# Performance work log

Measured on AMD Instinct MI355X. Metric: run time of the kernel, lower is better.

The kernel has to match this reference:

```python
import jax, jax.numpy as jnp
import numpy as np

PI_APPROX = 3.14  # the original module uses 3.14, not math.pi
FPS = 30.0        # hard-coded sampling rate in calc_hr_torch


def setup_inputs() -> dict:
    key = jax.random.key(0)
    x = jax.random.normal(key, (4096, 4096), dtype=jnp.float32)
    return {"x": x}


def reference(x) -> jnp.ndarray:
    test_n, sig_length = x.shape
    # mean-subtract each signal (over last dim)
    x = x - jnp.mean(x, axis=-1, keepdims=True)

    # custom_fft: DFT over dim 0 (size test_n), O(N^2) via trig matmuls
    N = test_n
    n = jnp.arange(N, dtype=jnp.float32)[:, None]  # [N,1]
    k = jnp.arange(N, dtype=jnp.float32)[None, :]  # [1,N]
    ang = (-2.0 * PI_APPROX / N) * (k * n)         # [N,N]
    real_part = jnp.matmul(jnp.cos(ang), x)        # [N, sig_length]
    imag_part = jnp.matmul(jnp.sin(ang), x)

    # custom_rfft: keep non-negative frequencies along dim 0
    half = N // 2 + 1 if N % 2 == 0 else (N + 1) // 2
    real_part = real_part[:half]
    imag_part = imag_part[:half]

    Ns = sig_length
    freq = jnp.arange(Ns, dtype=jnp.float32) / (Ns / FPS)  # [sig_length]
    amplitude = jnp.sqrt(real_part ** 2 + imag_part ** 2) / Ns  # [half, sig_length]
    hr_list = freq[jnp.argmax(amplitude, axis=-1)] * 60.0       # [half]
    return hr_list
```

## Files before the change

kernel.cpp:

```cpp
#include <hip/hip_runtime.h>
#include <cmath>

typedef _Float16 f16;
typedef _Float16 f16x8 __attribute__((ext_vector_type(8)));
typedef float f32x4 __attribute__((ext_vector_type(4)));
typedef unsigned long long u64;

#define M_OUT 2049
#define NDIM 4096
#define MPAD 2112
#define CW ((float)(-2.0 * 3.14 / 4096.0))

static const size_t WS_MEAN  = 0;
static const size_t WS_CELLS = 16384;
static const size_t WS_TBL   = 40960;
static const size_t A_ELEMS  = (size_t)MPAD * NDIM;
static const size_t X_ELEMS  = (size_t)NDIM * NDIM;
static const size_t WS_XTBL  = WS_TBL + 4 * A_ELEMS * sizeof(f16);
static const size_t WS_FULL_END = WS_XTBL + 2 * X_ELEMS * sizeof(f16);
static const size_t WS_MID_END  = WS_TBL + 4 * A_ELEMS * sizeof(f16);

#define AS1 __attribute__((address_space(1)))
#define AS3 __attribute__((address_space(3)))
__device__ __forceinline__ void async_copy16(const void* gsrc, void* ldst) {
    __builtin_amdgcn_global_load_lds((const AS1 unsigned int*)gsrc,
                                     (AS3 unsigned int*)ldst, 16, 0, 0);
}

__device__ __forceinline__ void split_f16(float v, f16& hi, f16& lo) {
    hi = (f16)v;
    lo = (f16)((v - (float)hi) * 64.0f);
}

__global__ void mean_kernel(const float* __restrict__ x, float* __restrict__ meanv) {
    const int row = blockIdx.x;
    const float4* xr = (const float4*)(x + (size_t)row * NDIM);
    float s = 0.f;
    for (int i = threadIdx.x; i < NDIM / 4; i += 256) {
        float4 v = xr[i];
        s += (v.x + v.y) + (v.z + v.w);
    }
    for (int off = 32; off; off >>= 1) s += __shfl_down(s, off);
    __shared__ float ps[4];
    if ((threadIdx.x & 63) == 0) ps[threadIdx.x >> 6] = s;
    __syncthreads();
    if (threadIdx.x == 0) {
        float t = (ps[0] + ps[1]) + (ps[2] + ps[3]);
        meanv[row] = t * (1.0f / 4096.0f);
    }
}

__global__ void init_cells(u64* __restrict__ cells) {
    int i = blockIdx.x * 256 + threadIdx.x;
    if (i < M_OUT) cells[i] = 0ull;
}

__global__ void fill_A_cm(f16* __restrict__ tbl) {
    const int c = blockIdx.x;
    const int m = blockIdx.y * 256 + threadIdx.x;
    if (m >= MPAD) return;
    const bool valid = (m < M_OUT);
    f16x8 chv, clv, shv, slv;
    for (int j = 0; j < 8; ++j) {
        float cc = 0.f, ss = 0.f;
        if (valid) {
            int kk = c * 8 + j;
            float ang = CW * (float)(m * kk);
            sincosf(ang, &ss, &cc);
        }
        f16 h, l;
        split_f16(cc, h, l); chv[j] = h; clv[j] = l;
        split_f16(ss, h, l); shv[j] = h; slv[j] = l;
    }
    size_t idx = ((size_t)c * MPAD + m) * 8;
    *(f16x8*)(tbl + idx)                 = chv;
    *(f16x8*)(tbl + A_ELEMS + idx)       = clv;
    *(f16x8*)(tbl + 2 * A_ELEMS + idx)   = shv;
    *(f16x8*)(tbl + 3 * A_ELEMS + idx)   = slv;
}

__global__ void fill_X_cm(const float* __restrict__ x, const float* __restrict__ meanv,
                          f16* __restrict__ xtbl) {
    const int c = blockIdx.x;
    const int n = blockIdx.y * 256 + threadIdx.x;
    f16x8 hv, lv;
    for (int j = 0; j < 8; ++j) {
        int k = c * 8 + j;
        float v = x[(size_t)k * NDIM + n] - meanv[k];
        f16 h, l;
        split_f16(v, h, l);
        hv[j] = h; lv[j] = l;
    }
    size_t idx = ((size_t)c * NDIM + n) * 8;
    *(f16x8*)(xtbl + idx)           = hv;
    *(f16x8*)(xtbl + X_ELEMS + idx) = lv;
}

__global__ __launch_bounds__(256, 2) void dft_gemm_cm(
    const f16* __restrict__ atbl, const f16* __restrict__ xtbl,
    u64* __restrict__ cells)
{
    __shared__ alignas(16) f16 sX[2][2][4][128][8];

    const int t = threadIdx.x;
    const int n0      = blockIdx.x * 128;
    const int rowBase = blockIdx.y * 64;

    const int lane = t & 63;
    const int w  = t >> 6;
    const int wm = w >> 1, wn = w & 1;
    const int q  = lane >> 4, ln = lane & 15;

    f32x4 aC0[2][4], aC1[2][4], aS0[2][4], aS1[2][4];
#pragma unroll
    for (int i = 0; i < 2; ++i)
#pragma unroll
        for (int j = 0; j < 4; ++j) {
            aC0[i][j] = (f32x4){0.f, 0.f, 0.f, 0.f};
            aC1[i][j] = (f32x4){0.f, 0.f, 0.f, 0.f};
            aS0[i][j] = (f32x4){0.f, 0.f, 0.f, 0.f};
            aS1[i][j] = (f32x4){0.f, 0.f, 0.f, 0.f};
        }

    const f16* aBase = atbl + ((size_t)q * MPAD + (rowBase + wm * 32 + ln)) * 8;

    const int xq0 = w >> 1, xh = w & 1;
    const int xq1 = xq0 + 2;
    const f16* xG0 = xtbl + ((size_t)xq0 * NDIM + n0 + xh * 64 + lane) * 8;
    const f16* xG1 = xtbl + ((size_t)xq1 * NDIM + n0 + xh * 64 + lane) * 8;
    const f16* xG2 = xG0 + X_ELEMS;
    const f16* xG3 = xG1 + X_ELEMS;

    auto loadA = [&](f16x8 (&dst)[2][4], int kc) {
#pragma unroll
        for (int tm = 0; tm < 2; ++tm)
#pragma unroll
            for (int tb = 0; tb < 4; ++tb)
                dst[tm][tb] = *(const f16x8*)(aBase + (size_t)tb * A_ELEMS
                              + ((size_t)kc * MPAD + tm * 16) * 8);
    };

    auto stageX = [&](int buf, int kc) {
        const size_t kadv = (size_t)kc * NDIM * 8;
        async_copy16(xG0 + kadv, &sX[buf][0][xq0][xh * 64][0]);
        async_copy16(xG1 + kadv, &sX[buf][0][xq1][xh * 64][0]);
        async_copy16(xG2 + kadv, &sX[buf][1][xq0][xh * 64][0]);
        async_copy16(xG3 + kadv, &sX[buf][1][xq1][xh * 64][0]);
    };

    auto compute = [&](f16x8 (&A)[2][4], int buf) {
        f16x8 bh[4], bl[4];
#pragma unroll
        for (int tn = 0; tn < 4; ++tn) {
            int nl = wn * 64 + tn * 16 + ln;
            bh[tn] = *(const f16x8*)&sX[buf][0][q][nl][0];
            bl[tn] = *(const f16x8*)&sX[buf][1][q][nl][0];
        }
#pragma unroll
        for (int tm = 0; tm < 2; ++tm)
#pragma unroll
            for (int tn = 0; tn < 4; ++tn) {
                aC0[tm][tn] = __builtin_amdgcn_mfma_f32_16x16x32_f16(A[tm][0], bh[tn], aC0[tm][tn], 0, 0, 0);
                aC1[tm][tn] = __builtin_amdgcn_mfma_f32_16x16x32_f16(A[tm][0], bl[tn], aC1[tm][tn], 0, 0, 0);
                aC1[tm][tn] = __builtin_amdgcn_mfma_f32_16x16x32_f16(A[tm][1], bh[tn], aC1[tm][tn], 0, 0, 0);
                aS0[tm][tn] = __builtin_amdgcn_mfma_f32_16x16x32_f16(A[tm][2], bh[tn], aS0[tm][tn], 0, 0, 0);
                aS1[tm][tn] = __builtin_amdgcn_mfma_f32_16x16x32_f16(A[tm][2], bl[tn], aS1[tm][tn], 0, 0, 0);
                aS1[tm][tn] = __builtin_amdgcn_mfma_f32_16x16x32_f16(A[tm][3], bh[tn], aS1[tm][tn], 0, 0, 0);
            }
    };

    f16x8 Aa[2][4], Ab[2][4];
    loadA(Aa, 0);
    stageX(0, 0);
    for (int kc = 0; kc < 512; kc += 8) {
        __syncthreads();
        stageX(1, kc + 4);
        loadA(Ab, kc + 4);
        compute(Aa, 0);
        __syncthreads();
        if (kc + 8 < 512) {
            stageX(0, kc + 8);
            loadA(Aa, kc + 8);
        }
        compute(Ab, 1);
    }

    const float inv64 = 0.015625f;
#pragma unroll
    for (int tm = 0; tm < 2; ++tm) {
#pragma unroll
        for (int r = 0; r < 4; ++r) {
            u64 best = 0ull;
#pragma unroll
            for (int tn = 0; tn < 4; ++tn) {
                float C = aC0[tm][tn][r] + aC1[tm][tn][r] * inv64;
                float S = aS0[tm][tn][r] + aS1[tm][tn][r] * inv64;
                float a2 = C * C + S * S;
                int col = n0 + wn * 64 + tn * 16 + ln;
                u64 key = ((u64)__float_as_uint(a2) << 32) | (unsigned)(~col);
                if (key > best) best = key;
            }
            for (int off = 1; off < 16; off <<= 1) {
                unsigned hi = (unsigned)(best >> 32), lo = (unsigned)best;
                unsigned ho = __shfl_xor(hi, off);
                unsigned lo2 = __shfl_xor(lo, off);
                u64 o = ((u64)ho << 32) | lo2;
                if (o > best) best = o;
            }
            if (ln == 0) {
                int grow = rowBase + wm * 32 + tm * 16 + q * 4 + r;
                if (grow < M_OUT) atomicMax(cells + grow, best);
            }
        }
    }
}

__global__ void fill_tables_rm(f16* __restrict__ tbl) {
    long long g = (long long)blockIdx.x * 256 + threadIdx.x;
    if (g >= (long long)(MPAD * 512)) return;
    int m  = (int)(g >> 9);
    int kq = ((int)g & 511) * 8;
    bool valid = (m < M_OUT);
    f16x8 chv, clv, shv, slv;
    for (int j = 0; j < 8; ++j) {
        float c = 0.f, s = 0.f;
        if (valid) {
            int kk = kq + j;
            float ang = CW * (float)(m * kk);
            sincosf(ang, &s, &c);
        }
        f16 h, l;
        split_f16(c, h, l); chv[j] = h; clv[j] = l;
        split_f16(s, h, l); shv[j] = h; slv[j] = l;
    }
    size_t idx = (size_t)m * NDIM + kq;
    *(f16x8*)(tbl + idx)               = chv;
    *(f16x8*)(tbl + A_ELEMS + idx)     = clv;
    *(f16x8*)(tbl + 2 * A_ELEMS + idx) = shv;
    *(f16x8*)(tbl + 3 * A_ELEMS + idx) = slv;
}

#define PK 40
__global__ __launch_bounds__(256, 2) void dft_gemm_fb(
    const float* __restrict__ x, const float* __restrict__ meanv,
    const f16* __restrict__ tbl, int useTbl,
    u64* __restrict__ cells)
{
    __shared__ alignas(16) f16 Ach[64][PK];
    __shared__ alignas(16) f16 Acl[64][PK];
    __shared__ alignas(16) f16 Ash[64][PK];
    __shared__ alignas(16) f16 Asl[64][PK];
    __shared__ alignas(16) f16 Xh[128][PK];
    __shared__ alignas(16) f16 Xl[128][PK];

    const int t = threadIdx.x;
    const int n0      = blockIdx.x * 128;
    const int rowBase = blockIdx.y * 64;

    const int am  = t >> 2;
    const int akq = (t & 3) * 8;
    const int xn  = t & 127;
    const int xkh = (t >> 7) * 16;

    const int lane = t & 63;
    const int w  = t >> 6;
    const int wm = w >> 1, wn = w & 1;
    const int q  = lane >> 4, ln = lane & 15;

    f32x4 aC0[2][4], aC1[2][4], aS0[2][4], aS1[2][4];
    for (int i = 0; i < 2; ++i)
        for (int j = 0; j < 4; ++j) {
            aC0[i][j] = (f32x4){0.f, 0.f, 0.f, 0.f};
            aC1[i][j] = (f32x4){0.f, 0.f, 0.f, 0.f};
            aS0[i][j] = (f32x4){0.f, 0.f, 0.f, 0.f};
            aS1[i][j] = (f32x4){0.f, 0.f, 0.f, 0.f};
        }

    const int arow = rowBase + am;
    const bool avalid = (arow < M_OUT);

    for (int k0 = 0; k0 < NDIM; k0 += 32) {
        __syncthreads();
        if (useTbl) {
            size_t idx = (size_t)arow * NDIM + k0 + akq;
            *(f16x8*)&Ach[am][akq] = *(const f16x8*)(tbl + idx);
            *(f16x8*)&Acl[am][akq] = *(const f16x8*)(tbl + A_ELEMS + idx);
            *(f16x8*)&Ash[am][akq] = *(const f16x8*)(tbl + 2 * A_ELEMS + idx);
            *(f16x8*)&Asl[am][akq] = *(const f16x8*)(tbl + 3 * A_ELEMS + idx);
        } else {
            f16x8 chv, clv, shv, slv;
            for (int j = 0; j < 8; ++j) {
                float c = 0.f, s = 0.f;
                if (avalid) {
                    int kk = k0 + akq + j;
                    float ang = CW * (float)(arow * kk);
                    sincosf(ang, &s, &c);
                }
                f16 h, l;
                split_f16(c, h, l); chv[j] = h; clv[j] = l;
                split_f16(s, h, l); shv[j] = h; slv[j] = l;
            }
            *(f16x8*)&Ach[am][akq] = chv;
            *(f16x8*)&Acl[am][akq] = clv;
            *(f16x8*)&Ash[am][akq] = shv;
            *(f16x8*)&Asl[am][akq] = slv;
        }
        {
            const float* xp = x + (size_t)(k0 + xkh) * NDIM + n0 + xn;
            f16x8 h0, h1, l0, l1;
            for (int r = 0; r < 16; ++r) {
                float v = xp[(size_t)r * NDIM] - meanv[k0 + xkh + r];
                f16 hi, lo;
                split_f16(v, hi, lo);
                if (r < 8) { h0[r] = hi; l0[r] = lo; }
                else       { h1[r - 8] = hi; l1[r - 8] = lo; }
            }
            *(f16x8*)&Xh[xn][xkh]     = h0;
            *(f16x8*)&Xh[xn][xkh + 8] = h1;
            *(f16x8*)&Xl[xn][xkh]     = l0;
            *(f16x8*)&Xl[xn][xkh + 8] = l1;
        }
        __syncthreads();
        f16x8 fch[2], fcl[2], fsh[2], fsl[2], bh[4], bl[4];
        for (int tm = 0; tm < 2; ++tm) {
            int ml = wm * 32 + tm * 16 + ln;
            fch[tm] = *(const f16x8*)&Ach[ml][q * 8];
            fcl[tm] = *(const f16x8*)&Acl[ml][q * 8];
            fsh[tm] = *(const f16x8*)&Ash[ml][q * 8];
            fsl[tm] = *(const f16x8*)&Asl[ml][q * 8];
        }
        for (int tn = 0; tn < 4; ++tn) {
            int nl = wn * 64 + tn * 16 + ln;
            bh[tn] = *(const f16x8*)&Xh[nl][q * 8];
            bl[tn] = *(const f16x8*)&Xl[nl][q * 8];
        }
        for (int tm = 0; tm < 2; ++tm)
            for (int tn = 0; tn < 4; ++tn) {
                aC0[tm][tn] = __builtin_amdgcn_mfma_f32_16x16x32_f16(fch[tm], bh[tn], aC0[tm][tn], 0, 0, 0);
                aC1[tm][tn] = __builtin_amdgcn_mfma_f32_16x16x32_f16(fch[tm], bl[tn], aC1[tm][tn], 0, 0, 0);
                aC1[tm][tn] = __builtin_amdgcn_mfma_f32_16x16x32_f16(fcl[tm], bh[tn], aC1[tm][tn], 0, 0, 0);
                aS0[tm][tn] = __builtin_amdgcn_mfma_f32_16x16x32_f16(fsh[tm], bh[tn], aS0[tm][tn], 0, 0, 0);
                aS1[tm][tn] = __builtin_amdgcn_mfma_f32_16x16x32_f16(fsh[tm], bl[tn], aS1[tm][tn], 0, 0, 0);
                aS1[tm][tn] = __builtin_amdgcn_mfma_f32_16x16x32_f16(fsl[tm], bh[tn], aS1[tm][tn], 0, 0, 0);
            }
    }

    const float inv64 = 0.015625f;
    for (int tm = 0; tm < 2; ++tm) {
        for (int r = 0; r < 4; ++r) {
            u64 best = 0ull;
            for (int tn = 0; tn < 4; ++tn) {
                float C = aC0[tm][tn][r] + aC1[tm][tn][r] * inv64;
                float S = aS0[tm][tn][r] + aS1[tm][tn][r] * inv64;
                float a2 = C * C + S * S;
                int col = n0 + wn * 64 + tn * 16 + ln;
                u64 key = ((u64)__float_as_uint(a2) << 32) | (unsigned)(~col);
                if (key > best) best = key;
            }
            for (int off = 1; off < 16; off <<= 1) {
                unsigned hi = (unsigned)(best >> 32), lo = (unsigned)best;
                unsigned ho = __shfl_xor(hi, off);
                unsigned lo2 = __shfl_xor(lo, off);
                u64 o = ((u64)ho << 32) | lo2;
                if (o > best) best = o;
            }
            if (ln == 0) {
                int grow = rowBase + wm * 32 + tm * 16 + q * 4 + r;
                if (grow < M_OUT) atomicMax(cells + grow, best);
            }
        }
    }
}

__global__ void out_kernel(const u64* __restrict__ cells, float* __restrict__ out) {
    int i = blockIdx.x * 256 + threadIdx.x;
    if (i < M_OUT) {
        unsigned col = ~(unsigned)(cells[i] & 0xFFFFFFFFull);
        float freq = (float)col / (4096.0f / 30.0f);
        out[i] = freq * 60.0f;
    }
}

extern "C" void kernel_launch(void* const* d_in, const int* in_sizes, int n_in,
                              void* d_out, int out_size, void* d_ws, size_t ws_size,
                              hipStream_t stream) {
    const float* x = (const float*)d_in[0];
    char* ws = (char*)d_ws;
    float* meanv = (float*)(ws + WS_MEAN);
    u64*   cells = (u64*)(ws + WS_CELLS);
    f16*   atbl  = (f16*)(ws + WS_TBL);
    f16*   xtbl  = (f16*)(ws + WS_XTBL);
    float* out   = (float*)d_out;

    hipLaunchKernelGGL(init_cells, dim3((M_OUT + 255) / 256), dim3(256), 0, stream, cells);
    hipLaunchKernelGGL(mean_kernel, dim3(NDIM), dim3(256), 0, stream, x, meanv);

    if (ws_size >= WS_FULL_END) {
        hipLaunchKernelGGL(fill_A_cm, dim3(512, 9), dim3(256), 0, stream, atbl);
        hipLaunchKernelGGL(fill_X_cm, dim3(512, 16), dim3(256), 0, stream, x, meanv, xtbl);
        hipLaunchKernelGGL(dft_gemm_cm, dim3(32, 33), dim3(256), 0, stream, atbl, xtbl, cells);
    } else if (ws_size >= WS_MID_END) {
        hipLaunchKernelGGL(fill_tables_rm, dim3(4224), dim3(256), 0, stream, atbl);
        hipLaunchKernelGGL(dft_gemm_fb, dim3(32, 33), dim3(256), 0, stream,
                           x, meanv, atbl, 1, cells);
    } else {
        hipLaunchKernelGGL(dft_gemm_fb, dim3(32, 33), dim3(256), 0, stream,
                           x, meanv, atbl, 0, cells);
    }
    hipLaunchKernelGGL(out_kernel, dim3((M_OUT + 255) / 256), dim3(256), 0, stream, cells, out);
}
```

Measured before the change: 533.0 us.

## Triple-buffer X tiles with partial vmcnt waits and raise MFMA priority

Moves the shared-memory X staging from a double buffer to a rotating triple buffer. Each step issues the next global A and X loads, then waits only until the previous stage's loads have landed (vmcnt 12), so a single barrier per step replaces the two full syncthreads. MFMA sections are wrapped in s_setprio to favour the matrix work. This grows LDS use by half, which could limit occupancy at two blocks per CU, and the hand-counted vmcnt value must match the number of outstanding loads exactly or the kernel reads stale data.

```diff
diff --git a/kernel.cpp b/kernel.cpp
--- a/kernel.cpp
+++ b/kernel.cpp
@@ -100,7 +100,7 @@
     const f16* __restrict__ atbl, const f16* __restrict__ xtbl,
     u64* __restrict__ cells)
 {
-    __shared__ alignas(16) f16 sX[2][2][4][128][8];
+    __shared__ alignas(16) f16 sX[3][2][4][128][8];
 
     const int t = threadIdx.x;
     const int n0      = blockIdx.x * 128;
@@ -156,6 +156,7 @@
             bh[tn] = *(const f16x8*)&sX[buf][0][q][nl][0];
             bl[tn] = *(const f16x8*)&sX[buf][1][q][nl][0];
         }
+        __builtin_amdgcn_s_setprio(1);
 #pragma unroll
         for (int tm = 0; tm < 2; ++tm)
 #pragma unroll
@@ -167,23 +168,46 @@
                 aS1[tm][tn] = __builtin_amdgcn_mfma_f32_16x16x32_f16(A[tm][2], bl[tn], aS1[tm][tn], 0, 0, 0);
                 aS1[tm][tn] = __builtin_amdgcn_mfma_f32_16x16x32_f16(A[tm][3], bh[tn], aS1[tm][tn], 0, 0, 0);
             }
+        __builtin_amdgcn_s_setprio(0);
     };
 
     f16x8 Aa[2][4], Ab[2][4];
+    int cur = 0, nxt = 1;
+    auto bump = [&]() { cur = nxt; nxt = (nxt == 2) ? 0 : nxt + 1; };
+
+    stageX(0, 0);
     loadA(Aa, 0);
-    stageX(0, 0);
-    for (int kc = 0; kc < 512; kc += 8) {
-        __syncthreads();
-        stageX(1, kc + 4);
+
+    int kc = 0;
+    for (int it = 0; it < 63; ++it) {
         loadA(Ab, kc + 4);
-        compute(Aa, 0);
-        __syncthreads();
-        if (kc + 8 < 512) {
-            stageX(0, kc + 8);
-            loadA(Aa, kc + 8);
-        }
-        compute(Ab, 1);
-    }
+        stageX(nxt, kc + 4);
+        asm volatile("s_waitcnt vmcnt(12)" ::: "memory");
+        __builtin_amdgcn_s_barrier();
+        __builtin_amdgcn_sched_barrier(0);
+        compute(Aa, cur);
+        bump();
+        kc += 4;
+        loadA(Aa, kc + 4);
+        stageX(nxt, kc + 4);
+        asm volatile("s_waitcnt vmcnt(12)" ::: "memory");
+        __builtin_amdgcn_s_barrier();
+        __builtin_amdgcn_sched_barrier(0);
+        compute(Ab, cur);
+        bump();
+        kc += 4;
+    }
+    loadA(Ab, kc + 4);
+    stageX(nxt, kc + 4);
+    asm volatile("s_waitcnt vmcnt(12)" ::: "memory");
+    __builtin_amdgcn_s_barrier();
+    __builtin_amdgcn_sched_barrier(0);
+    compute(Aa, cur);
+    bump();
+    asm volatile("s_waitcnt vmcnt(0)" ::: "memory");
+    __builtin_amdgcn_s_barrier();
+    __builtin_amdgcn_sched_barrier(0);
+    compute(Ab, cur);
 
     const float inv64 = 0.015625f;
 #pragma unroll
```

New measurement: 533.5 us. No clear change (+0.1%).

## Give each wave a private X tile and drop block barriers in DFT GEMM loop

Applied to the files above, without the earlier changes.

Each wave now loads its own copy of the X slice it consumes into wave-private shared memory, so the __syncthreads barriers in the main loop can be removed. Explicit vmcnt waits and sched_barriers replace them, and the last iteration is peeled out of the loop. s_setprio is raised around the MFMA block. The cost is duplicated X traffic (waves with the same wn stage identical data) and double the LDS footprint, which may reduce occupancy.

```diff
diff --git a/kernel.cpp b/kernel.cpp
--- a/kernel.cpp
+++ b/kernel.cpp
@@ -100,7 +100,7 @@
     const f16* __restrict__ atbl, const f16* __restrict__ xtbl,
     u64* __restrict__ cells)
 {
-    __shared__ alignas(16) f16 sX[2][2][4][128][8];
+    __shared__ alignas(16) f16 sX[2][4][2][4][64][8];
 
     const int t = threadIdx.x;
     const int n0      = blockIdx.x * 128;
@@ -124,12 +124,7 @@
 
     const f16* aBase = atbl + ((size_t)q * MPAD + (rowBase + wm * 32 + ln)) * 8;
 
-    const int xq0 = w >> 1, xh = w & 1;
-    const int xq1 = xq0 + 2;
-    const f16* xG0 = xtbl + ((size_t)xq0 * NDIM + n0 + xh * 64 + lane) * 8;
-    const f16* xG1 = xtbl + ((size_t)xq1 * NDIM + n0 + xh * 64 + lane) * 8;
-    const f16* xG2 = xG0 + X_ELEMS;
-    const f16* xG3 = xG1 + X_ELEMS;
+    const f16* xBase = xtbl + (size_t)(n0 + wn * 64 + lane) * 8;
 
     auto loadA = [&](f16x8 (&dst)[2][4], int kc) {
 #pragma unroll
@@ -141,21 +136,23 @@
     };
 
     auto stageX = [&](int buf, int kc) {
-        const size_t kadv = (size_t)kc * NDIM * 8;
-        async_copy16(xG0 + kadv, &sX[buf][0][xq0][xh * 64][0]);
-        async_copy16(xG1 + kadv, &sX[buf][0][xq1][xh * 64][0]);
-        async_copy16(xG2 + kadv, &sX[buf][1][xq0][xh * 64][0]);
-        async_copy16(xG3 + kadv, &sX[buf][1][xq1][xh * 64][0]);
+        const f16* src = xBase + (size_t)kc * (NDIM * 8);
+#pragma unroll
+        for (int tb = 0; tb < 2; ++tb)
+#pragma unroll
+            for (int p = 0; p < 4; ++p)
+                async_copy16(src + (size_t)tb * X_ELEMS + (size_t)p * (NDIM * 8),
+                             &sX[buf][w][tb][p][0][0]);
     };
 
     auto compute = [&](f16x8 (&A)[2][4], int buf) {
         f16x8 bh[4], bl[4];
 #pragma unroll
         for (int tn = 0; tn < 4; ++tn) {
-            int nl = wn * 64 + tn * 16 + ln;
-            bh[tn] = *(const f16x8*)&sX[buf][0][q][nl][0];
-            bl[tn] = *(const f16x8*)&sX[buf][1][q][nl][0];
-        }
+            bh[tn] = *(const f16x8*)&sX[buf][w][0][q][tn * 16 + ln][0];
+            bl[tn] = *(const f16x8*)&sX[buf][w][1][q][tn * 16 + ln][0];
+        }
+        __builtin_amdgcn_s_setprio(1);
 #pragma unroll
         for (int tm = 0; tm < 2; ++tm)
 #pragma unroll
@@ -167,23 +164,38 @@
                 aS1[tm][tn] = __builtin_amdgcn_mfma_f32_16x16x32_f16(A[tm][2], bl[tn], aS1[tm][tn], 0, 0, 0);
                 aS1[tm][tn] = __builtin_amdgcn_mfma_f32_16x16x32_f16(A[tm][3], bh[tn], aS1[tm][tn], 0, 0, 0);
             }
+        __builtin_amdgcn_s_setprio(0);
     };
 
     f16x8 Aa[2][4], Ab[2][4];
+
     loadA(Aa, 0);
     stageX(0, 0);
-    for (int kc = 0; kc < 512; kc += 8) {
-        __syncthreads();
+
+    for (int i = 0; i < 63; ++i) {
+        const int kc = i * 8;
+        __builtin_amdgcn_sched_barrier(0);
+        loadA(Ab, kc + 4);
         stageX(1, kc + 4);
-        loadA(Ab, kc + 4);
+        asm volatile("s_waitcnt vmcnt(16)" ::: "memory");
+        __builtin_amdgcn_sched_barrier(0);
         compute(Aa, 0);
-        __syncthreads();
-        if (kc + 8 < 512) {
-            stageX(0, kc + 8);
-            loadA(Aa, kc + 8);
-        }
+        __builtin_amdgcn_sched_barrier(0);
+        loadA(Aa, kc + 8);
+        stageX(0, kc + 8);
+        asm volatile("s_waitcnt vmcnt(16)" ::: "memory");
+        __builtin_amdgcn_sched_barrier(0);
         compute(Ab, 1);
     }
+    __builtin_amdgcn_sched_barrier(0);
+    loadA(Ab, 508);
+    stageX(1, 508);
+    asm volatile("s_waitcnt vmcnt(16)" ::: "memory");
+    __builtin_amdgcn_sched_barrier(0);
+    compute(Aa, 0);
+    asm volatile("s_waitcnt vmcnt(0)" ::: "memory");
+    __builtin_amdgcn_sched_barrier(0);
+    compute(Ab, 1);
 
     const float inv64 = 0.015625f;
 #pragma unroll
```

Result: slower. 579.0 us (+8.6%).
